# Performance work log

Measured on AMD Instinct MI355X. Metric: run time of the kernel, lower is better.

## Reference

```python
import jax, jax.numpy as jnp
import numpy as np

B, S, D, H = 4, 2048, 1024, 16
HD = D // H  # head_dim = 64


def setup_inputs() -> dict:
    key = jax.random.key(0)
    ks = jax.random.split(key, 5)
    hidden_states = jax.random.normal(ks[0], (B, S, D), dtype=jnp.float32)
    # GPT-2 Conv1D: out = x @ W + b, W shape [in, out]
    w_attn = jax.random.normal(ks[1], (D, 3 * D), dtype=jnp.float32) * 0.02
    b_attn = jnp.zeros((3 * D,), dtype=jnp.float32)
    w_proj = jax.random.normal(ks[2], (D, D), dtype=jnp.float32) * 0.02
    b_proj = jnp.zeros((D,), dtype=jnp.float32)
    return {"hidden_states": hidden_states, "w_attn": w_attn, "b_attn": b_attn,
            "w_proj": w_proj, "b_proj": b_proj}


def reference(hidden_states, w_attn, b_attn, w_proj, b_proj):
    b, s, d = hidden_states.shape
    qkv = hidden_states @ w_attn + b_attn                     # [B,S,3D]
    q, k, v = jnp.split(qkv, 3, axis=-1)
    # split heads -> [B,H,S,HD]
    def heads(x):
        return x.reshape(b, s, H, HD).transpose(0, 2, 1, 3)
    q, k, v = heads(q), heads(k), heads(v)
    # scaled dot product; GPT-2 divides by sqrt(head_dim)
    scores = jnp.einsum("bhqd,bhkd->bhqk", q, k) / jnp.sqrt(jnp.float32(HD))
    causal = jnp.tril(jnp.ones((s, s), dtype=bool))           # [S,S]
    neg = jnp.finfo(scores.dtype).min
    scores = jnp.where(causal[None, None, :, :], scores, neg)
    attn = jax.nn.softmax(scores, axis=-1)
    ctx = jnp.einsum("bhqk,bhkd->bhqd", attn, v)              # [B,H,S,HD]
    ctx = ctx.transpose(0, 2, 1, 3).reshape(b, s, d)          # merge heads
    return ctx @ w_proj + b_proj
```

## Files before the change

### kernel.cpp

```cpp
#include <hip/hip_runtime.h>
#include <hip/hip_bf16.h>

typedef __bf16 bf16;
typedef bf16 bf16x8 __attribute__((ext_vector_type(8)));
typedef bf16 bf16x4 __attribute__((ext_vector_type(4)));
typedef float f32x4 __attribute__((ext_vector_type(4)));
typedef float f32x16 __attribute__((ext_vector_type(16)));
typedef unsigned int uint2v __attribute__((ext_vector_type(2)));

#define MFMA16(a, b, c) __builtin_amdgcn_mfma_f32_16x16x32_bf16(a, b, c, 0, 0, 0)
#define MFMA32(a, b, c) __builtin_amdgcn_mfma_f32_32x32x16_bf16(a, b, c, 0, 0, 0)

constexpr int Bn = 4, Sn = 2048, Dn = 1024, Hn = 16, HDn = 64;
constexpr int Mn = Bn * Sn;

__device__ __forceinline__ bf16x8 cvt8(float4 a, float4 b) {
  bf16x8 v = {(bf16)a.x, (bf16)a.y, (bf16)a.z, (bf16)a.w,
              (bf16)b.x, (bf16)b.y, (bf16)b.z, (bf16)b.w};
  return v;
}

__device__ __forceinline__ void load_lds16(const bf16* g, bf16* l) {
  __builtin_amdgcn_global_load_lds(
      (const __attribute__((address_space(1))) void*)g,
      (__attribute__((address_space(3))) void*)l, 16, 0, 0);
}

__device__ __forceinline__ unsigned cvt_pk_bf16(float lo, float hi) {
  unsigned r;
  asm("v_cvt_pk_bf16_f32 %0, %1, %2" : "=v"(r) : "v"(lo), "v"(hi));
  return r;
}

__global__ __launch_bounds__(256) void k_prep(const float* __restrict__ hidden,
                                              const float* __restrict__ w_attn,
                                              const float* __restrict__ w_proj,
                                              bf16* __restrict__ Xb,
                                              bf16* __restrict__ wattnT,
                                              bf16* __restrict__ wprojT) {
  __shared__ alignas(16) bf16 t[64][72];
  const int bx = blockIdx.x;
  const int tid = threadIdx.x;
  if (bx < 4096) {
    int i = bx * 256 + tid;
    const float4* p = (const float4*)hidden + (size_t)i * 2;
    float4 a = p[0], b = p[1];
    *((bf16x8*)Xb + i) = cvt8(a, b);
    return;
  }
  const float* in;
  bf16* out;
  int K = 1024, N, n0, k0;
  if (bx < 4864) {
    int idx = bx - 4096;
    in = w_attn; out = wattnT; N = 3072;
    n0 = (idx % 48) * 64; k0 = (idx / 48) * 64;
  } else {
    int idx = bx - 4864;
    in = w_proj; out = wprojT; N = 1024;
    n0 = (idx % 16) * 64; k0 = (idx / 16) * 64;
  }
  {
    int row = tid >> 2;
    int c16 = (tid & 3) * 16;
    const float* src = in + (size_t)(k0 + row) * N + n0 + c16;
    float4 f0 = ((const float4*)src)[0];
    float4 f1 = ((const float4*)src)[1];
    float4 f2 = ((const float4*)src)[2];
    float4 f3 = ((const float4*)src)[3];
    *(bf16x8*)&t[row][c16] = cvt8(f0, f1);
    *(bf16x8*)&t[row][c16 + 8] = cvt8(f2, f3);
  }
  __syncthreads();
#pragma unroll
  for (int i = 0; i < 2; i++) {
    int c = tid + i * 256;
    int nrow = c >> 3, kcol8 = (c & 7) * 8;
    bf16x8 v;
#pragma unroll
    for (int j = 0; j < 8; j++) v[j] = t[kcol8 + j][nrow];
    *(bf16x8*)(out + (size_t)(n0 + nrow) * K + k0 + kcol8) = v;
  }
}


__global__ __launch_bounds__(256) void k_gemm_qkv(const bf16* __restrict__ A,
                                                  const bf16* __restrict__ BT,
                                                  const float* __restrict__ bias,
                                                  bf16* __restrict__ Qo,
                                                  bf16* __restrict__ Ko,
                                                  bf16* __restrict__ Vt) {
  __shared__ alignas(16) bf16 la[128 * 32];
  __shared__ alignas(16) bf16 lb[128 * 32];
  const int tid = threadIdx.x;
  const int w = tid >> 6, lane = tid & 63, l15 = lane & 15, quad = lane >> 4;
  const int wm = w >> 1, wn = w & 1;
  const int m0 = blockIdx.y * 128, n0 = blockIdx.x * 128;
  const int lrow = lane >> 2, lcol = (lane & 3) * 8;

  f32x4 acc[4][4];
#pragma unroll
  for (int i = 0; i < 4; i++)
#pragma unroll
    for (int j = 0; j < 4; j++) acc[i][j] = f32x4{0.f, 0.f, 0.f, 0.f};

  for (int k0 = 0; k0 < 1024; k0 += 32) {
    __syncthreads();
    load_lds16(A + (size_t)(m0 + w * 16 + lrow) * 1024 + k0 + lcol, &la[w * 512]);
    load_lds16(A + (size_t)(m0 + 64 + w * 16 + lrow) * 1024 + k0 + lcol, &la[(w + 4) * 512]);
    load_lds16(BT + (size_t)(n0 + w * 16 + lrow) * 1024 + k0 + lcol, &lb[w * 512]);
    load_lds16(BT + (size_t)(n0 + 64 + w * 16 + lrow) * 1024 + k0 + lcol, &lb[(w + 4) * 512]);
    __syncthreads();
    bf16x8 af[4], bfr[4];
#pragma unroll
    for (int i = 0; i < 4; i++)
      af[i] = *(const bf16x8*)&la[(wm * 64 + i * 16 + l15) * 32 + quad * 8];
#pragma unroll
    for (int j = 0; j < 4; j++)
      bfr[j] = *(const bf16x8*)&lb[(wn * 64 + j * 16 + l15) * 32 + quad * 8];
#pragma unroll
    for (int i = 0; i < 4; i++)
#pragma unroll
      for (int j = 0; j < 4; j++) acc[i][j] = MFMA16(af[i], bfr[j], acc[i][j]);
  }

#pragma unroll
  for (int j = 0; j < 4; j++) {
    int ng = n0 + wn * 64 + j * 16 + l15;
    float bs = bias[ng];
    int which = ng >> 10;
    int nloc = ng & 1023, hh = nloc >> 6, hd = nloc & 63;
#pragma unroll
    for (int i = 0; i < 4; i++) {
      int mg0 = m0 + wm * 64 + i * 16 + quad * 4;
      int bb = mg0 >> 11, ss = mg0 & 2047;
      if (which == 2) {
        bf16x4 v;
#pragma unroll
        for (int r = 0; r < 4; r++) v[r] = (bf16)(acc[i][j][r] + bs);
        *(bf16x4*)&Vt[((size_t)(bb * Hn + hh) * HDn + hd) * Sn + ss] = v;
      } else {
        bf16* dst = which ? Ko : Qo;
#pragma unroll
        for (int r = 0; r < 4; r++)
          dst[((size_t)(bb * Hn + hh) * Sn + ss + r) * HDn + hd] =
              (bf16)(acc[i][j][r] + bs);
      }
    }
  }
}

__global__ __launch_bounds__(256) void k_gemm_proj(const bf16* __restrict__ A,
                                                   const bf16* __restrict__ BT,
                                                   const float* __restrict__ bias,
                                                   float* __restrict__ out) {
  __shared__ alignas(16) bf16 la[128 * 32];
  __shared__ alignas(16) bf16 lb[128 * 32];
  const int tid = threadIdx.x;
  const int w = tid >> 6, lane = tid & 63, l15 = lane & 15, quad = lane >> 4;
  const int wm = w >> 1, wn = w & 1;
  const int m0 = blockIdx.y * 128, n0 = blockIdx.x * 128;
  const int lrow = lane >> 2, lcol = (lane & 3) * 8;

  f32x4 acc[4][4];
#pragma unroll
  for (int i = 0; i < 4; i++)
#pragma unroll
    for (int j = 0; j < 4; j++) acc[i][j] = f32x4{0.f, 0.f, 0.f, 0.f};

  for (int k0 = 0; k0 < 1024; k0 += 32) {
    __syncthreads();
    load_lds16(A + (size_t)(m0 + w * 16 + lrow) * 1024 + k0 + lcol, &la[w * 512]);
    load_lds16(A + (size_t)(m0 + 64 + w * 16 + lrow) * 1024 + k0 + lcol, &la[(w + 4) * 512]);
    load_lds16(BT + (size_t)(n0 + w * 16 + lrow) * 1024 + k0 + lcol, &lb[w * 512]);
    load_lds16(BT + (size_t)(n0 + 64 + w * 16 + lrow) * 1024 + k0 + lcol, &lb[(w + 4) * 512]);
    __syncthreads();
    bf16x8 af[4], bfr[4];
#pragma unroll
    for (int i = 0; i < 4; i++)
      af[i] = *(const bf16x8*)&la[(wm * 64 + i * 16 + l15) * 32 + quad * 8];
#pragma unroll
    for (int j = 0; j < 4; j++)
      bfr[j] = *(const bf16x8*)&lb[(wn * 64 + j * 16 + l15) * 32 + quad * 8];
#pragma unroll
    for (int i = 0; i < 4; i++)
#pragma unroll
      for (int j = 0; j < 4; j++) acc[i][j] = MFMA16(af[i], bfr[j], acc[i][j]);
  }

#pragma unroll
  for (int j = 0; j < 4; j++) {
    int ng = n0 + wn * 64 + j * 16 + l15;
    float bs = bias[ng];
#pragma unroll
    for (int i = 0; i < 4; i++) {
      int mg0 = m0 + wm * 64 + i * 16 + quad * 4;
#pragma unroll
      for (int r = 0; r < 4; r++)
        out[(size_t)(mg0 + r) * 1024 + ng] = acc[i][j][r] + bs;
    }
  }
}

__global__ __launch_bounds__(256) void k_attn(const bf16* __restrict__ Q,
                                              const bf16* __restrict__ Kv,
                                              const bf16* __restrict__ Vtg,
                                              bf16* __restrict__ ctx) {
  __shared__ alignas(16) bf16 kl[3][64 * 64];
  __shared__ alignas(16) bf16 vl[3][64 * 64];

  const int bh = blockIdx.x;
  const int qt = 15 - blockIdx.y;
  const int bb = bh >> 4, hh = bh & 15;
  const int tid = threadIdx.x;
  const int w = tid >> 6, lane = tid & 63, l31 = lane & 31, hi = lane >> 5;
  const size_t base = (size_t)bh * Sn * HDn;
  const int q0 = qt * 128 + w * 32;
  const int nt = 2 * qt + 2;

  const int r0 = tid >> 3, s0 = tid & 7;
  const int ksw = (s0 ^ (r0 & 7)) << 3;
  const bf16* Krow = Kv + base + (size_t)r0 * 64 + ksw;
  const bf16* Vrow0 = Vtg + ((size_t)bh * 64 + r0) * Sn + ksw;
  const bf16* Vrow1 = Vtg + ((size_t)bh * 64 + r0 + 32) * Sn + ksw;
  const int sw7 = l31 & 7;

  bf16x8 qf[4];
#pragma unroll
  for (int c = 0; c < 4; c++) {
    bf16x8 v = *(const bf16x8*)(Q + base + (size_t)(q0 + l31) * 64 + c * 16 + hi * 8);
#pragma unroll
    for (int e = 0; e < 8; e++) v[e] = (bf16)((float)v[e] * 0.125f);
    qf[c] = v;
  }

  f32x16 o0, o1;
#pragma unroll
  for (int e = 0; e < 16; e++) { o0[e] = 0.f; o1[e] = 0.f; }
  float dsum = 0.f;

#define STAGE(t_, bf_)                                                  \
  {                                                                     \
    const int kb_ = (t_) * 64;                                          \
    load_lds16(Krow + (size_t)kb_ * 64, &kl[bf_][w * 512]);             \
    load_lds16(Krow + (size_t)(kb_ + 32) * 64, &kl[bf_][2048 + w * 512]); \
    load_lds16(Vrow0 + kb_, &vl[bf_][w * 512]);                         \
    load_lds16(Vrow1 + kb_, &vl[bf_][2048 + w * 512]);                  \
  }

  STAGE(0, 0)
  STAGE(1, 1)

  int cb = 0, sb = 2;
  for (int t = 0; t < nt; ++t) {
    if (t == nt - 1) asm volatile("s_waitcnt vmcnt(0)" ::: "memory");
    else             asm volatile("s_waitcnt vmcnt(4)" ::: "memory");
    __builtin_amdgcn_s_barrier();
    if (t + 2 < nt) STAGE(t + 2, sb)
    const int kb = t * 64;
    if (kb <= q0 + 31) {
      const bf16* klc = kl[cb];
      const bf16* vlc = vl[cb];
#pragma unroll
      for (int sub = 0; sub < 2; sub++) {
        const int ks0 = kb + sub * 32;
        if (ks0 > q0 + 31) break;
        f32x16 st;
#pragma unroll
        for (int e = 0; e < 16; e++) st[e] = 0.f;
#pragma unroll
        for (int c = 0; c < 4; c++) {
          const int row = sub * 32 + l31;
          bf16x8 kf = *(const bf16x8*)&klc[row * 64 + (((2 * c + hi) ^ sw7) << 3)];
          st = MFMA32(kf, qf[c], st);
        }
        if (ks0 == q0) {
#pragma unroll
          for (int r = 0; r < 16; r++) {
            int krel = (r & 3) + 8 * (r >> 2) + 4 * hi;
            if (krel > l31) st[r] = -1e30f;
          }
        }
#pragma unroll
        for (int r = 0; r < 16; r++) {
          st[r] = __expf(st[r]);
          dsum += st[r];
        }
#pragma unroll
        for (int c2 = 0; c2 < 2; c2++) {
          unsigned wa0 = cvt_pk_bf16(st[8 * c2 + 0], st[8 * c2 + 1]);
          unsigned wa1 = cvt_pk_bf16(st[8 * c2 + 2], st[8 * c2 + 3]);
          unsigned wb0 = cvt_pk_bf16(st[8 * c2 + 4], st[8 * c2 + 5]);
          unsigned wb1 = cvt_pk_bf16(st[8 * c2 + 6], st[8 * c2 + 7]);
          unsigned pw0, pw1, pw2, pw3;
#if __has_builtin(__builtin_amdgcn_permlane32_swap)
          uint2v sw0 = __builtin_amdgcn_permlane32_swap(wa0, wb0, false, false);
          uint2v sw1 = __builtin_amdgcn_permlane32_swap(wa1, wb1, false, false);
          pw0 = sw0.x; pw1 = sw1.x; pw2 = sw0.y; pw3 = sw1.y;
#else
          unsigned xa0 = __shfl_xor((int)wa0, 32, 64), xb0 = __shfl_xor((int)wb0, 32, 64);
          unsigned xa1 = __shfl_xor((int)wa1, 32, 64), xb1 = __shfl_xor((int)wb1, 32, 64);
          pw0 = hi ? xb0 : wa0; pw1 = hi ? xb1 : wa1;
          pw2 = hi ? wb0 : xa0; pw3 = hi ? wb1 : xa1;
#endif
          union { unsigned u[4]; bf16x8 v; } pb;
          pb.u[0] = pw0; pb.u[1] = pw1; pb.u[2] = pw2; pb.u[3] = pw3;
          const int vs = sub * 4 + 2 * c2;
          bf16x8 vf0 = *(const bf16x8*)&vlc[l31 * 64 + (((vs + hi) ^ sw7) << 3)];
          o0 = MFMA32(vf0, pb.v, o0);
          bf16x8 vf1 = *(const bf16x8*)&vlc[(32 + l31) * 64 + (((vs + hi) ^ sw7) << 3)];
          o1 = MFMA32(vf1, pb.v, o1);
        }
      }
    }
    cb = (cb == 2) ? 0 : cb + 1;
    sb = (sb == 2) ? 0 : sb + 1;
  }
#undef STAGE

  float tot = dsum + __shfl_xor(dsum, 32, 64);
  float inv = 1.f / fmaxf(tot, 1e-20f);
  size_t ob = ((size_t)(bb * Sn + q0 + l31)) * Dn + hh * HDn + hi * 4;
#pragma unroll
  for (int g = 0; g < 4; g++) {
    bf16x4 v0, v1;
#pragma unroll
    for (int r = 0; r < 4; r++) {
      v0[r] = (bf16)(o0[4 * g + r] * inv);
      v1[r] = (bf16)(o1[4 * g + r] * inv);
    }
    *(bf16x4*)&ctx[ob + g * 8] = v0;
    *(bf16x4*)&ctx[ob + 32 + g * 8] = v1;
  }
}

extern "C" void kernel_launch(void* const* d_in, const int* in_sizes, int n_in,
                              void* d_out, int out_size, void* d_ws, size_t ws_size,
                              hipStream_t stream) {
  const float* hidden = (const float*)d_in[0];
  const float* w_attn = (const float*)d_in[1];
  const float* b_attn = (const float*)d_in[2];
  const float* w_proj = (const float*)d_in[3];
  const float* b_proj = (const float*)d_in[4];
  float* out = (float*)d_out;

  bf16* ws = (bf16*)d_ws;
  const size_t QKV_ELEMS = (size_t)Bn * Hn * Sn * HDn;
  bf16* Qb = ws;
  bf16* Kb = Qb + QKV_ELEMS;
  bf16* Vt = Kb + QKV_ELEMS;
  bf16* ctx = Vt + QKV_ELEMS;
  bf16* Xb = ctx;
  bf16* wattnT = ctx + (size_t)Mn * Dn;
  bf16* wprojT = wattnT + (size_t)Dn * 3 * Dn;

  k_prep<<<5120, 256, 0, stream>>>(hidden, w_attn, w_proj, Xb, wattnT, wprojT);
  k_gemm_qkv<<<dim3(24, 64), 256, 0, stream>>>(Xb, wattnT, b_attn, Qb, Kb, Vt);
  k_attn<<<dim3(64, 16), 256, 0, stream>>>(Qb, Kb, Vt, ctx);
  k_gemm_proj<<<dim3(8, 64), 256, 0, stream>>>(ctx, wprojT, b_proj, out);
}
```

Before: 241.3 us.

## Triple-buffer GEMM LDS tiles with async prefetch and XOR swizzle

Both the QKV and output-projection GEMMs now use three LDS buffers per operand and prefetch tiles two k-steps ahead. Each step waits on vmcnt with a single barrier instead of two __syncthreads per step. An XOR swizzle is applied to the column offset on the global-to-LDS copy and on the fragment reads to reduce LDS bank conflicts. The aim is to overlap global loads with MFMA work, at the cost of triple the LDS per block, which may lower occupancy.

```diff
diff --git a/kernel.cpp b/kernel.cpp
--- a/kernel.cpp
+++ b/kernel.cpp
@@ -90,13 +90,15 @@
                                                   bf16* __restrict__ Qo,
                                                   bf16* __restrict__ Ko,
                                                   bf16* __restrict__ Vt) {
-  __shared__ alignas(16) bf16 la[128 * 32];
-  __shared__ alignas(16) bf16 lb[128 * 32];
+  __shared__ alignas(16) bf16 la[3][128 * 32];
+  __shared__ alignas(16) bf16 lb[3][128 * 32];
   const int tid = threadIdx.x;
   const int w = tid >> 6, lane = tid & 63, l15 = lane & 15, quad = lane >> 4;
   const int wm = w >> 1, wn = w & 1;
   const int m0 = blockIdx.y * 128, n0 = blockIdx.x * 128;
-  const int lrow = lane >> 2, lcol = (lane & 3) * 8;
+  const int lrow = lane >> 2;
+  const int scol = ((lane & 3) ^ (lrow & 3)) * 8;
+  const int rs3 = l15 & 3;
 
   f32x4 acc[4][4];
 #pragma unroll
@@ -104,25 +106,46 @@
 #pragma unroll
     for (int j = 0; j < 4; j++) acc[i][j] = f32x4{0.f, 0.f, 0.f, 0.f};
 
-  for (int k0 = 0; k0 < 1024; k0 += 32) {
-    __syncthreads();
-    load_lds16(A + (size_t)(m0 + w * 16 + lrow) * 1024 + k0 + lcol, &la[w * 512]);
-    load_lds16(A + (size_t)(m0 + 64 + w * 16 + lrow) * 1024 + k0 + lcol, &la[(w + 4) * 512]);
-    load_lds16(BT + (size_t)(n0 + w * 16 + lrow) * 1024 + k0 + lcol, &lb[w * 512]);
-    load_lds16(BT + (size_t)(n0 + 64 + w * 16 + lrow) * 1024 + k0 + lcol, &lb[(w + 4) * 512]);
-    __syncthreads();
+#define STAGEQ(t_, bf_)                                                          \
+  {                                                                              \
+    const int kk = (t_) * 32;                                                    \
+    load_lds16(A + (size_t)(m0 + w * 16 + lrow) * 1024 + kk + scol,              \
+               &la[bf_][w * 512]);                                               \
+    load_lds16(A + (size_t)(m0 + 64 + w * 16 + lrow) * 1024 + kk + scol,         \
+               &la[bf_][(w + 4) * 512]);                                         \
+    load_lds16(BT + (size_t)(n0 + w * 16 + lrow) * 1024 + kk + scol,             \
+               &lb[bf_][w * 512]);                                               \
+    load_lds16(BT + (size_t)(n0 + 64 + w * 16 + lrow) * 1024 + kk + scol,        \
+               &lb[bf_][(w + 4) * 512]);                                         \
+  }
+
+  STAGEQ(0, 0)
+  STAGEQ(1, 1)
+  int cb = 0, sb = 2;
+  for (int t = 0; t < 32; ++t) {
+    if (t == 31) asm volatile("s_waitcnt vmcnt(0)" ::: "memory");
+    else         asm volatile("s_waitcnt vmcnt(4)" ::: "memory");
+    __builtin_amdgcn_s_barrier();
+    if (t + 2 < 32) STAGEQ(t + 2, sb)
+    const bf16* lac = la[cb];
+    const bf16* lbc = lb[cb];
     bf16x8 af[4], bfr[4];
 #pragma unroll
     for (int i = 0; i < 4; i++)
-      af[i] = *(const bf16x8*)&la[(wm * 64 + i * 16 + l15) * 32 + quad * 8];
+      af[i] = *(const bf16x8*)&lac[(wm * 64 + i * 16 + l15) * 32 +
+                                   ((quad ^ rs3) << 3)];
 #pragma unroll
     for (int j = 0; j < 4; j++)
-      bfr[j] = *(const bf16x8*)&lb[(wn * 64 + j * 16 + l15) * 32 + quad * 8];
+      bfr[j] = *(const bf16x8*)&lbc[(wn * 64 + j * 16 + l15) * 32 +
+                                    ((quad ^ rs3) << 3)];
 #pragma unroll
     for (int i = 0; i < 4; i++)
 #pragma unroll
       for (int j = 0; j < 4; j++) acc[i][j] = MFMA16(af[i], bfr[j], acc[i][j]);
-  }
+    cb = (cb == 2) ? 0 : cb + 1;
+    sb = (sb == 2) ? 0 : sb + 1;
+  }
+#undef STAGEQ
 
 #pragma unroll
   for (int j = 0; j < 4; j++) {
@@ -154,13 +177,15 @@
                                                    const bf16* __restrict__ BT,
                                                    const float* __restrict__ bias,
                                                    float* __restrict__ out) {
-  __shared__ alignas(16) bf16 la[128 * 32];
-  __shared__ alignas(16) bf16 lb[128 * 32];
+  __shared__ alignas(16) bf16 la[3][128 * 32];
+  __shared__ alignas(16) bf16 lb[3][128 * 32];
   const int tid = threadIdx.x;
   const int w = tid >> 6, lane = tid & 63, l15 = lane & 15, quad = lane >> 4;
   const int wm = w >> 1, wn = w & 1;
   const int m0 = blockIdx.y * 128, n0 = blockIdx.x * 128;
-  const int lrow = lane >> 2, lcol = (lane & 3) * 8;
+  const int lrow = lane >> 2;
+  const int scol = ((lane & 3) ^ (lrow & 3)) * 8;
+  const int rs3 = l15 & 3;
 
   f32x4 acc[4][4];
 #pragma unroll
@@ -168,25 +193,46 @@
 #pragma unroll
     for (int j = 0; j < 4; j++) acc[i][j] = f32x4{0.f, 0.f, 0.f, 0.f};
 
-  for (int k0 = 0; k0 < 1024; k0 += 32) {
-    __syncthreads();
-    load_lds16(A + (size_t)(m0 + w * 16 + lrow) * 1024 + k0 + lcol, &la[w * 512]);
-    load_lds16(A + (size_t)(m0 + 64 + w * 16 + lrow) * 1024 + k0 + lcol, &la[(w + 4) * 512]);
-    load_lds16(BT + (size_t)(n0 + w * 16 + lrow) * 1024 + k0 + lcol, &lb[w * 512]);
-    load_lds16(BT + (size_t)(n0 + 64 + w * 16 + lrow) * 1024 + k0 + lcol, &lb[(w + 4) * 512]);
-    __syncthreads();
+#define STAGEP(t_, bf_)                                                          \
+  {                                                                              \
+    const int kk = (t_) * 32;                                                    \
+    load_lds16(A + (size_t)(m0 + w * 16 + lrow) * 1024 + kk + scol,              \
+               &la[bf_][w * 512]);                                               \
+    load_lds16(A + (size_t)(m0 + 64 + w * 16 + lrow) * 1024 + kk + scol,         \
+               &la[bf_][(w + 4) * 512]);                                         \
+    load_lds16(BT + (size_t)(n0 + w * 16 + lrow) * 1024 + kk + scol,             \
+               &lb[bf_][w * 512]);                                               \
+    load_lds16(BT + (size_t)(n0 + 64 + w * 16 + lrow) * 1024 + kk + scol,        \
+               &lb[bf_][(w + 4) * 512]);                                         \
+  }
+
+  STAGEP(0, 0)
+  STAGEP(1, 1)
+  int cb = 0, sb = 2;
+  for (int t = 0; t < 32; ++t) {
+    if (t == 31) asm volatile("s_waitcnt vmcnt(0)" ::: "memory");
+    else         asm volatile("s_waitcnt vmcnt(4)" ::: "memory");
+    __builtin_amdgcn_s_barrier();
+    if (t + 2 < 32) STAGEP(t + 2, sb)
+    const bf16* lac = la[cb];
+    const bf16* lbc = lb[cb];
     bf16x8 af[4], bfr[4];
 #pragma unroll
     for (int i = 0; i < 4; i++)
-      af[i] = *(const bf16x8*)&la[(wm * 64 + i * 16 + l15) * 32 + quad * 8];
+      af[i] = *(const bf16x8*)&lac[(wm * 64 + i * 16 + l15) * 32 +
+                                   ((quad ^ rs3) << 3)];
 #pragma unroll
     for (int j = 0; j < 4; j++)
-      bfr[j] = *(const bf16x8*)&lb[(wn * 64 + j * 16 + l15) * 32 + quad * 8];
+      bfr[j] = *(const bf16x8*)&lbc[(wn * 64 + j * 16 + l15) * 32 +
+                                    ((quad ^ rs3) << 3)];
 #pragma unroll
     for (int i = 0; i < 4; i++)
 #pragma unroll
       for (int j = 0; j < 4; j++) acc[i][j] = MFMA16(af[i], bfr[j], acc[i][j]);
-  }
+    cb = (cb == 2) ? 0 : cb + 1;
+    sb = (sb == 2) ? 0 : sb + 1;
+  }
+#undef STAGEP
 
 #pragma unroll
   for (int j = 0; j < 4; j++) {
```

Result: slower. 255.2 us (+5.7%).

## Triple-buffer LDS in QKV and projection GEMMs to overlap loads with MFMA

Applied to the files above, without the earlier changes.

Both GEMM kernels move from a single LDS buffer with two barriers per k-step to a three-stage ring. Asynchronous global-to-LDS loads for the tile two steps ahead are issued while MFMAs consume the current tile, with manual vmcnt waits and one barrier per step. This is meant to hide global load latency and cut synchronisation, at the cost of three times the LDS per block, which may reduce occupancy.

```diff
diff --git a/kernel.cpp b/kernel.cpp
--- a/kernel.cpp
+++ b/kernel.cpp
@@ -90,39 +90,65 @@
                                                   bf16* __restrict__ Qo,
                                                   bf16* __restrict__ Ko,
                                                   bf16* __restrict__ Vt) {
-  __shared__ alignas(16) bf16 la[128 * 32];
-  __shared__ alignas(16) bf16 lb[128 * 32];
+  __shared__ alignas(16) bf16 la[3][128 * 32];
+  __shared__ alignas(16) bf16 lb[3][128 * 32];
   const int tid = threadIdx.x;
   const int w = tid >> 6, lane = tid & 63, l15 = lane & 15, quad = lane >> 4;
   const int wm = w >> 1, wn = w & 1;
   const int m0 = blockIdx.y * 128, n0 = blockIdx.x * 128;
   const int lrow = lane >> 2, lcol = (lane & 3) * 8;
 
+  const bf16* a0 = A + (size_t)(m0 + w * 16 + lrow) * 1024 + lcol;
+  const bf16* a1 = A + (size_t)(m0 + 64 + w * 16 + lrow) * 1024 + lcol;
+  const bf16* b0 = BT + (size_t)(n0 + w * 16 + lrow) * 1024 + lcol;
+  const bf16* b1 = BT + (size_t)(n0 + 64 + w * 16 + lrow) * 1024 + lcol;
+
   f32x4 acc[4][4];
 #pragma unroll
   for (int i = 0; i < 4; i++)
 #pragma unroll
     for (int j = 0; j < 4; j++) acc[i][j] = f32x4{0.f, 0.f, 0.f, 0.f};
 
-  for (int k0 = 0; k0 < 1024; k0 += 32) {
-    __syncthreads();
-    load_lds16(A + (size_t)(m0 + w * 16 + lrow) * 1024 + k0 + lcol, &la[w * 512]);
-    load_lds16(A + (size_t)(m0 + 64 + w * 16 + lrow) * 1024 + k0 + lcol, &la[(w + 4) * 512]);
-    load_lds16(BT + (size_t)(n0 + w * 16 + lrow) * 1024 + k0 + lcol, &lb[w * 512]);
-    load_lds16(BT + (size_t)(n0 + 64 + w * 16 + lrow) * 1024 + k0 + lcol, &lb[(w + 4) * 512]);
-    __syncthreads();
-    bf16x8 af[4], bfr[4];
-#pragma unroll
-    for (int i = 0; i < 4; i++)
-      af[i] = *(const bf16x8*)&la[(wm * 64 + i * 16 + l15) * 32 + quad * 8];
-#pragma unroll
-    for (int j = 0; j < 4; j++)
-      bfr[j] = *(const bf16x8*)&lb[(wn * 64 + j * 16 + l15) * 32 + quad * 8];
-#pragma unroll
-    for (int i = 0; i < 4; i++)
-#pragma unroll
-      for (int j = 0; j < 4; j++) acc[i][j] = MFMA16(af[i], bfr[j], acc[i][j]);
-  }
+#define STAGEQ(kk_, bf_)                                   \
+  {                                                        \
+    load_lds16(a0 + (kk_), &la[bf_][w * 512]);             \
+    load_lds16(a1 + (kk_), &la[bf_][(w + 4) * 512]);       \
+    load_lds16(b0 + (kk_), &lb[bf_][w * 512]);             \
+    load_lds16(b1 + (kk_), &lb[bf_][(w + 4) * 512]);       \
+  }
+
+#define PHASEQ(cb_, sb_, kk_, dostage_, last_)                                 \
+  {                                                                            \
+    if (last_) asm volatile("s_waitcnt vmcnt(0)" ::: "memory");                \
+    else       asm volatile("s_waitcnt vmcnt(4)" ::: "memory");                \
+    __builtin_amdgcn_s_barrier();                                              \
+    if (dostage_) STAGEQ((kk_) + 64, sb_)                                      \
+    bf16x8 af[4], bfr[4];                                                      \
+    _Pragma("unroll")                                                          \
+    for (int i = 0; i < 4; i++)                                                \
+      af[i] = *(const bf16x8*)&la[cb_][(wm * 64 + i * 16 + l15) * 32 +         \
+                                       quad * 8];                              \
+    _Pragma("unroll")                                                          \
+    for (int j = 0; j < 4; j++)                                                \
+      bfr[j] = *(const bf16x8*)&lb[cb_][(wn * 64 + j * 16 + l15) * 32 +        \
+                                        quad * 8];                             \
+    _Pragma("unroll")                                                          \
+    for (int i = 0; i < 4; i++)                                                \
+      _Pragma("unroll")                                                        \
+      for (int j = 0; j < 4; j++) acc[i][j] = MFMA16(af[i], bfr[j], acc[i][j]); \
+  }
+
+  STAGEQ(0, 0)
+  STAGEQ(32, 1)
+  for (int kk = 0; kk < 30 * 32; kk += 96) {
+    PHASEQ(0, 2, kk, 1, 0)
+    PHASEQ(1, 0, kk + 32, 1, 0)
+    PHASEQ(2, 1, kk + 64, 1, 0)
+  }
+  PHASEQ(0, 2, 30 * 32, 0, 0)
+  PHASEQ(1, 0, 31 * 32, 0, 1)
+#undef PHASEQ
+#undef STAGEQ
 
 #pragma unroll
   for (int j = 0; j < 4; j++) {
@@ -154,39 +180,65 @@
                                                    const bf16* __restrict__ BT,
                                                    const float* __restrict__ bias,
                                                    float* __restrict__ out) {
-  __shared__ alignas(16) bf16 la[128 * 32];
-  __shared__ alignas(16) bf16 lb[128 * 32];
+  __shared__ alignas(16) bf16 la[3][128 * 32];
+  __shared__ alignas(16) bf16 lb[3][128 * 32];
   const int tid = threadIdx.x;
   const int w = tid >> 6, lane = tid & 63, l15 = lane & 15, quad = lane >> 4;
   const int wm = w >> 1, wn = w & 1;
   const int m0 = blockIdx.y * 128, n0 = blockIdx.x * 128;
   const int lrow = lane >> 2, lcol = (lane & 3) * 8;
 
+  const bf16* a0 = A + (size_t)(m0 + w * 16 + lrow) * 1024 + lcol;
+  const bf16* a1 = A + (size_t)(m0 + 64 + w * 16 + lrow) * 1024 + lcol;
+  const bf16* b0 = BT + (size_t)(n0 + w * 16 + lrow) * 1024 + lcol;
+  const bf16* b1 = BT + (size_t)(n0 + 64 + w * 16 + lrow) * 1024 + lcol;
+
   f32x4 acc[4][4];
 #pragma unroll
   for (int i = 0; i < 4; i++)
 #pragma unroll
     for (int j = 0; j < 4; j++) acc[i][j] = f32x4{0.f, 0.f, 0.f, 0.f};
 
-  for (int k0 = 0; k0 < 1024; k0 += 32) {
-    __syncthreads();
-    load_lds16(A + (size_t)(m0 + w * 16 + lrow) * 1024 + k0 + lcol, &la[w * 512]);
-    load_lds16(A + (size_t)(m0 + 64 + w * 16 + lrow) * 1024 + k0 + lcol, &la[(w + 4) * 512]);
-    load_lds16(BT + (size_t)(n0 + w * 16 + lrow) * 1024 + k0 + lcol, &lb[w * 512]);
-    load_lds16(BT + (size_t)(n0 + 64 + w * 16 + lrow) * 1024 + k0 + lcol, &lb[(w + 4) * 512]);
-    __syncthreads();
-    bf16x8 af[4], bfr[4];
-#pragma unroll
-    for (int i = 0; i < 4; i++)
-      af[i] = *(const bf16x8*)&la[(wm * 64 + i * 16 + l15) * 32 + quad * 8];
-#pragma unroll
-    for (int j = 0; j < 4; j++)
-      bfr[j] = *(const bf16x8*)&lb[(wn * 64 + j * 16 + l15) * 32 + quad * 8];
-#pragma unroll
-    for (int i = 0; i < 4; i++)
-#pragma unroll
-      for (int j = 0; j < 4; j++) acc[i][j] = MFMA16(af[i], bfr[j], acc[i][j]);
-  }
+#define STAGEP(kk_, bf_)                                   \
+  {                                                        \
+    load_lds16(a0 + (kk_), &la[bf_][w * 512]);             \
+    load_lds16(a1 + (kk_), &la[bf_][(w + 4) * 512]);       \
+    load_lds16(b0 + (kk_), &lb[bf_][w * 512]);             \
+    load_lds16(b1 + (kk_), &lb[bf_][(w + 4) * 512]);       \
+  }
+
+#define PHASEP(cb_, sb_, kk_, dostage_, last_)                                 \
+  {                                                                            \
+    if (last_) asm volatile("s_waitcnt vmcnt(0)" ::: "memory");                \
+    else       asm volatile("s_waitcnt vmcnt(4)" ::: "memory");                \
+    __builtin_amdgcn_s_barrier();                                              \
+    if (dostage_) STAGEP((kk_) + 64, sb_)                                      \
+    bf16x8 af[4], bfr[4];                                                      \
+    _Pragma("unroll")                                                          \
+    for (int i = 0; i < 4; i++)                                                \
+      af[i] = *(const bf16x8*)&la[cb_][(wm * 64 + i * 16 + l15) * 32 +         \
+                                       quad * 8];                              \
+    _Pragma("unroll")                                                          \
+    for (int j = 0; j < 4; j++)                                                \
+      bfr[j] = *(const bf16x8*)&lb[cb_][(wn * 64 + j * 16 + l15) * 32 +        \
+                                        quad * 8];                             \
+    _Pragma("unroll")                                                          \
+    for (int i = 0; i < 4; i++)                                                \
+      _Pragma("unroll")                                                        \
+      for (int j = 0; j < 4; j++) acc[i][j] = MFMA16(af[i], bfr[j], acc[i][j]); \
+  }
+
+  STAGEP(0, 0)
+  STAGEP(32, 1)
+  for (int kk = 0; kk < 30 * 32; kk += 96) {
+    PHASEP(0, 2, kk, 1, 0)
+    PHASEP(1, 0, kk + 32, 1, 0)
+    PHASEP(2, 1, kk + 64, 1, 0)
+  }
+  PHASEP(0, 2, 30 * 32, 0, 0)
+  PHASEP(1, 0, 31 * 32, 0, 1)
+#undef PHASEP
+#undef STAGEP
 
 #pragma unroll
   for (int j = 0; j < 4; j++) {
```

After: 257.6 us. 6.8% more time.
